# Optimization experiments

Hardware: AMD Instinct MI355X
Metric: run time of the kernel (lower is better)

Reference implementation:

```python
import jax, jax.numpy as jnp
import numpy as np

D = 512   # block_hidden_dim (also per-head dim in this module)
H = 8     # n_head
EPS_RENORM = 1e-13
LN_EPS = 1e-5

def setup_inputs() -> dict:
    key = jax.random.key(0)
    ks = jax.random.split(key, 10)
    B, L = 4, 1024
    std = np.sqrt(2.0 / (D * 2)).astype(np.float32)
    q = jax.random.normal(ks[0], (B, L, D), jnp.float32)
    k = jax.random.normal(ks[1], (B, L, D), jnp.float32)
    v = jax.random.normal(ks[2], (B, L, D), jnp.float32)
    mask = jax.random.randint(ks[3], (B, L, L), 0, 2, jnp.int32)
    Wq = jax.random.normal(ks[4], (H * D, D), jnp.float32) * std
    Wk = jax.random.normal(ks[5], (H * D, D), jnp.float32) * std
    Wv = jax.random.normal(ks[6], (H * D, D), jnp.float32) * std
    Wfc = jax.random.normal(ks[7], (D, H * D), jnp.float32) * np.sqrt(2.0 / (D + H * D)).astype(np.float32)
    bfc = jnp.zeros((D,), jnp.float32)
    gamma = jnp.ones((D,), jnp.float32)
    beta = jnp.zeros((D,), jnp.float32)
    return {"q": q, "mask": mask, "k": k, "v": v, "Wq": Wq, "Wk": Wk,
            "Wv": Wv, "Wfc": Wfc, "bfc": bfc, "gamma": gamma, "beta": beta}

def reference(q, mask, k, v, Wq, Wk, Wv, Wfc, bfc, gamma, beta):
    B, Lq, _ = q.shape
    residual = q
    # torch Linear: y = x @ W.T ; W reshaped to [H, D_out, D_in]
    qh = jnp.einsum('bqd,hed->bhqe', q, Wq.reshape(H, D, D))
    kh = jnp.einsum('bkd,hed->bhke', k, Wk.reshape(H, D, D))
    vh = jnp.einsum('bkd,hed->bhke', v, Wv.reshape(H, D, D))
    scores = jnp.einsum('bhqe,bhke->bhqk', qh, kh) / jnp.sqrt(jnp.float32(D))
    m = mask.astype(scores.dtype)[:, None, :, :]        # [B,1,Lq,Lk]
    # multiplicative-mask softmax + renormalization (allennlp masked_softmax)
    attn = jax.nn.softmax(scores * m, axis=-1)
    attn = attn * m
    attn = attn / (attn.sum(axis=-1, keepdims=True) + EPS_RENORM)
    out = jnp.einsum('bhqk,bhke->bhqe', attn, vh)       # [B,H,Lq,D]
    out = out.transpose(0, 2, 1, 3).reshape(B, Lq, H * D)  # head-major concat
    out = out @ Wfc.T + bfc                              # fc (dropout = eval no-op)
    x = out + residual
    mu = x.mean(axis=-1, keepdims=True)
    var = x.var(axis=-1, keepdims=True)
    out = (x - mu) / jnp.sqrt(var + LN_EPS) * gamma + beta
    attn_mean = attn.mean(axis=1)                        # mean over heads [B,Lq,Lk]
    return out, attn_mean
```

## Files before the change

### kernel.cpp

```cpp
#include <hip/hip_runtime.h>
#include <hip/hip_bf16.h>
#include <cmath>

typedef long long i64;
typedef unsigned short u16;
typedef __attribute__((ext_vector_type(8))) short short8;
typedef __attribute__((ext_vector_type(8))) unsigned short u16x8;
typedef __attribute__((ext_vector_type(4))) float f32x4;
typedef __attribute__((ext_vector_type(4))) int i32x4;

#define NB 4
#define NL 1024
#define ND 512
#define NH 8

__device__ __forceinline__ u16 f2bf(float f) {
    __hip_bfloat16 h = __float2bfloat16(f);
    return __builtin_bit_cast(unsigned short, h);
}
__device__ __forceinline__ float bf2f(u16 u) {
    return __builtin_bit_cast(float, (unsigned)u << 16);
}

typedef __attribute__((address_space(3))) u16* lds_u16p;
typedef const __attribute__((address_space(1))) u16* glb_u16p;
__device__ __forceinline__ void gl_lds16(const u16* g, u16* l) {
    __builtin_amdgcn_global_load_lds((glb_u16p)g, (lds_u16p)l, 16, 0, 0);
}

struct CvtArgs {
    const float* src[4];
    u16* dst[4];
};

__global__ __launch_bounds__(256) void cvt_multi_kernel(CvtArgs args, int n8)
{
    int i = blockIdx.x * 256 + threadIdx.x;
    if (i >= n8) return;
    const float* __restrict__ src = args.src[blockIdx.y];
    u16* __restrict__ dst = args.dst[blockIdx.y];
    float4 a = ((const float4*)src)[2 * i];
    float4 b = ((const float4*)src)[2 * i + 1];
    u16x8 o;
    o[0] = f2bf(a.x); o[1] = f2bf(a.y); o[2] = f2bf(a.z); o[3] = f2bf(a.w);
    o[4] = f2bf(b.x); o[5] = f2bf(b.y); o[6] = f2bf(b.z); o[7] = f2bf(b.w);
    *(u16x8*)&dst[8 * i] = o;
}

template <bool OUTBF, bool BIAS>
__global__ __launch_bounds__(256) void mfma_gemm(
    const u16* __restrict__ A, const u16* __restrict__ B,
    void* __restrict__ Cv, const float* __restrict__ bias,
    int K, int lda, int ldb, int ldc, float alpha,
    i64 a_s1, i64 a_s2, i64 b_s1, i64 b_s2, i64 c_s1, i64 c_s2)
{
    const int gxy  = gridDim.x * gridDim.y;
    const int nblk = gxy * gridDim.z;
    const int lin  = blockIdx.x + gridDim.x * blockIdx.y + gxy * blockIdx.z;
    const int swz  = (lin & 7) * (nblk >> 3) + (lin >> 3);
    const int bz   = swz / gxy;
    const int rxy  = swz - bz * gxy;
    const int by   = rxy / gridDim.x;
    const int bx   = rxy - by * gridDim.x;

    const int zh = bz >> 3, zl = bz & 7;
    A += (i64)zh * a_s1 + (i64)zl * a_s2;
    B += (i64)zh * b_s1 + (i64)zl * b_s2;
    const i64 coff = (i64)zh * c_s1 + (i64)zl * c_s2;

    __shared__ alignas(16) u16 As[128 * 64];
    __shared__ alignas(16) u16 Bs[128 * 64];

    const int tid  = threadIdx.x;
    const int lane = tid & 63;
    const int wave = tid >> 6;
    const int wr   = (wave >> 1) * 64;
    const int wc   = (wave & 1) * 64;
    const int lrow = lane & 15;
    const int kblk = lane >> 4;
    const int rsw  = (lrow & 7) * 8;
    const int m0   = by * 128;
    const int n0   = bx * 128;

    const int srow0 = wave * 32;
    const int lrel  = lane >> 3;
    const int grow  = srow0 + lrel;
    const int gchk  = ((lane & 7) ^ lrel) * 8;

    f32x4 acc[4][4];
    #pragma unroll
    for (int i = 0; i < 4; ++i)
        #pragma unroll
        for (int j = 0; j < 4; ++j)
            acc[i][j] = (f32x4){0.f, 0.f, 0.f, 0.f};

    for (int k0 = 0; k0 < K; k0 += 64) {
        #pragma unroll
        for (int j = 0; j < 4; ++j)
            gl_lds16(&A[(i64)(m0 + grow + 8 * j) * lda + k0 + gchk],
                     &As[(srow0 + 8 * j) * 64]);
        #pragma unroll
        for (int j = 0; j < 4; ++j)
            gl_lds16(&B[(i64)(n0 + grow + 8 * j) * ldb + k0 + gchk],
                     &Bs[(srow0 + 8 * j) * 64]);
        __syncthreads();

        #pragma unroll
        for (int kk = 0; kk < 2; ++kk) {
            short8 af[4], bg[4];
            #pragma unroll
            for (int m = 0; m < 4; ++m)
                af[m] = *(const short8*)&As[(wr + m * 16 + lrow) * 64 +
                                            (((kk * 32) + kblk * 8) ^ rsw)];
            #pragma unroll
            for (int n = 0; n < 4; ++n)
                bg[n] = *(const short8*)&Bs[(wc + n * 16 + lrow) * 64 +
                                            (((kk * 32) + kblk * 8) ^ rsw)];

            #pragma unroll
            for (int m = 0; m < 4; ++m)
                #pragma unroll
                for (int n = 0; n < 4; ++n)
                    acc[m][n] = __builtin_amdgcn_mfma_f32_16x16x32_bf16(
                        af[m], bg[n], acc[m][n], 0, 0, 0);
        }
        __syncthreads();
    }

    #pragma unroll
    for (int m = 0; m < 4; ++m) {
        #pragma unroll
        for (int n = 0; n < 4; ++n) {
            const int col = n0 + wc + n * 16 + lrow;
            float bv = BIAS ? bias[col] : 0.f;
            #pragma unroll
            for (int r = 0; r < 4; ++r) {
                const int row = m0 + wr + m * 16 + kblk * 4 + r;
                float val = acc[m][n][r] * alpha + bv;
                if (OUTBF)
                    ((u16*)Cv)[coff + (i64)row * ldc + col] = f2bf(val);
                else
                    ((float*)Cv)[coff + (i64)row * ldc + col] = val;
            }
        }
    }
}

template <int P>
__global__ __launch_bounds__(256) void reduce_fc_kernel(
    const float* __restrict__ part, const float* __restrict__ bias,
    float* __restrict__ outp, i64 pstride)
{
    i64 idx = (i64)blockIdx.x * 256 + threadIdx.x;
    float s = bias[idx & (ND - 1)];
    #pragma unroll
    for (int p = 0; p < P; ++p) s += part[(i64)p * pstride + idx];
    outp[idx] = s;
}

__device__ __forceinline__ float wave_red_sum(float v) {
    #pragma unroll
    for (int o = 32; o > 0; o >>= 1) v += __shfl_down(v, o, 64);
    return v;
}
__device__ __forceinline__ float wave_red_max(float v) {
    #pragma unroll
    for (int o = 32; o > 0; o >>= 1) v = fmaxf(v, __shfl_down(v, o, 64));
    return v;
}

__global__ __launch_bounds__(256) void softmax_fused_kernel(
    const u16* __restrict__ scores, const int* __restrict__ mask,
    u16* __restrict__ attn_bf, float* __restrict__ amean,
    i64 s_bstride, i64 m_bstride, i64 a_bstride, i64 o_bstride)
{
    const int qrow = blockIdx.x;
    const int bb   = blockIdx.y;
    const u16* sbase = scores + (i64)bb * s_bstride;
    const int* mrow = mask + (i64)bb * m_bstride + (i64)qrow * NL;
    u16* abase = attn_bf + (i64)bb * a_bstride;
    float* orow = amean + (i64)bb * o_bstride + (i64)qrow * NL;

    const int tid  = threadIdx.x;
    const int lane = tid & 63;
    const int wave = tid >> 6;

    __shared__ float wsum[4][NL];

    const int e0 = lane * 8;
    const int e1 = 512 + lane * 8;

    float mv[16];
    {
        i32x4 m0a = *(const i32x4*)&mrow[e0];
        i32x4 m0b = *(const i32x4*)&mrow[e0 + 4];
        i32x4 m1a = *(const i32x4*)&mrow[e1];
        i32x4 m1b = *(const i32x4*)&mrow[e1 + 4];
        #pragma unroll
        for (int i = 0; i < 4; ++i) {
            mv[i]      = (float)m0a[i];
            mv[4 + i]  = (float)m0b[i];
            mv[8 + i]  = (float)m1a[i];
            mv[12 + i] = (float)m1b[i];
        }
    }

    float msum[16];
    #pragma unroll
    for (int i = 0; i < 16; ++i) msum[i] = 0.f;

    #pragma unroll
    for (int hh = 0; hh < 2; ++hh) {
        const int h = wave + hh * 4;
        const u16* srow_p = sbase + ((i64)h * NL + qrow) * NL;
        u16* arow_p = abase + ((i64)h * NL + qrow) * NL;

        u16x8 s0 = *(const u16x8*)&srow_p[e0];
        u16x8 s1 = *(const u16x8*)&srow_p[e1];

        float zv[16];
        float lmax = -1e30f;
        #pragma unroll
        for (int i = 0; i < 8; ++i) {
            zv[i]     = bf2f(s0[i]) * mv[i];
            zv[8 + i] = bf2f(s1[i]) * mv[8 + i];
        }
        #pragma unroll
        for (int i = 0; i < 16; ++i) lmax = fmaxf(lmax, zv[i]);
        #pragma unroll
        for (int o = 1; o < 64; o <<= 1)
            lmax = fmaxf(lmax, __shfl_xor(lmax, o, 64));

        float e[16];
        float ls = 0.f;
        #pragma unroll
        for (int i = 0; i < 16; ++i) { e[i] = __expf(zv[i] - lmax); ls += e[i]; }
        #pragma unroll
        for (int o = 1; o < 64; o <<= 1) ls += __shfl_xor(ls, o, 64);

        float ls2 = 0.f;
        #pragma unroll
        for (int i = 0; i < 16; ++i) { e[i] = e[i] / ls * mv[i]; ls2 += e[i]; }
        #pragma unroll
        for (int o = 1; o < 64; o <<= 1) ls2 += __shfl_xor(ls2, o, 64);

        const float inv = 1.0f / (ls2 + 1e-13f);
        u16x8 o0, o1;
        #pragma unroll
        for (int i = 0; i < 8; ++i) {
            float p0 = e[i] * inv;
            float p1 = e[8 + i] * inv;
            o0[i] = f2bf(p0);
            o1[i] = f2bf(p1);
            msum[i]     += p0;
            msum[8 + i] += p1;
        }
        *(u16x8*)&arow_p[e0] = o0;
        *(u16x8*)&arow_p[e1] = o1;
    }

    #pragma unroll
    for (int i = 0; i < 8; ++i) {
        wsum[wave][e0 + i] = msum[i];
        wsum[wave][e1 + i] = msum[8 + i];
    }
    __syncthreads();
    #pragma unroll
    for (int i = 0; i < 4; ++i) {
        int j = tid + i * 256;
        orow[j] = (wsum[0][j] + wsum[1][j] + wsum[2][j] + wsum[3][j]) * 0.125f;
    }
}

__global__ __launch_bounds__(256) void ln_kernel(
    const float* __restrict__ fcout, const float* __restrict__ resid,
    const float* __restrict__ gamma, const float* __restrict__ beta,
    float* __restrict__ out)
{
    const int row = blockIdx.x;
    const float* xr = fcout + (i64)row * ND;
    const float* rr = resid + (i64)row * ND;
    const int tid = threadIdx.x;
    const int lane = tid & 63, wid = tid >> 6;
    __shared__ float red[8];

    float x0 = xr[tid] + rr[tid];
    float x1 = xr[tid + 256] + rr[tid + 256];
    float s  = x0 + x1;
    float s2 = x0 * x0 + x1 * x1;
    s  = wave_red_sum(s);
    s2 = wave_red_sum(s2);
    if (lane == 0) { red[wid] = s; red[4 + wid] = s2; }
    __syncthreads();
    const float S  = red[0] + red[1] + red[2] + red[3];
    const float S2 = red[4] + red[5] + red[6] + red[7];
    const float mu  = S * (1.0f / ND);
    const float var = S2 * (1.0f / ND) - mu * mu;
    const float inv = rsqrtf(var + 1e-5f);

    out[(i64)row * ND + tid]       = (x0 - mu) * inv * gamma[tid] + beta[tid];
    out[(i64)row * ND + tid + 256] = (x1 - mu) * inv * gamma[tid + 256] + beta[tid + 256];
}

template <bool BT, bool BIAS, bool ACC>
__global__ __launch_bounds__(256) void gemm_kernel(
    const float* __restrict__ A, const float* __restrict__ B,
    float* __restrict__ C, const float* __restrict__ bias,
    int M, int N, int K, int lda, int ldb, int ldc, float alpha)
{
    __shared__ float Asf[16][68];
    __shared__ float Bsf[16][68];
    const int tid = threadIdx.x;
    const int tx = tid & 15, ty = tid >> 4;
    const int m0 = blockIdx.y * 64, n0 = blockIdx.x * 64;
    float acc[4][4] = {};

    for (int k0 = 0; k0 < K; k0 += 16) {
        {
            int r = tid >> 2, kq = (tid & 3) << 2;
            float4 a = *reinterpret_cast<const float4*>(&A[(i64)(m0 + r) * lda + k0 + kq]);
            Asf[kq][r] = a.x; Asf[kq + 1][r] = a.y; Asf[kq + 2][r] = a.z; Asf[kq + 3][r] = a.w;
        }
        if (BT) {
            int r = tid >> 2, kq = (tid & 3) << 2;
            float4 b = *reinterpret_cast<const float4*>(&B[(i64)(n0 + r) * ldb + k0 + kq]);
            Bsf[kq][r] = b.x; Bsf[kq + 1][r] = b.y; Bsf[kq + 2][r] = b.z; Bsf[kq + 3][r] = b.w;
        } else {
            int kk = tid >> 4, n4 = (tid & 15) << 2;
            float4 b = *reinterpret_cast<const float4*>(&B[(i64)(k0 + kk) * ldb + n0 + n4]);
            *reinterpret_cast<float4*>(&Bsf[kk][n4]) = b;
        }
        __syncthreads();
        #pragma unroll
        for (int kk = 0; kk < 16; ++kk) {
            float4 a4 = *reinterpret_cast<const float4*>(&Asf[kk][ty << 2]);
            float4 b4 = *reinterpret_cast<const float4*>(&Bsf[kk][tx << 2]);
            float a[4] = {a4.x, a4.y, a4.z, a4.w};
            float b[4] = {b4.x, b4.y, b4.z, b4.w};
            #pragma unroll
            for (int i = 0; i < 4; ++i)
                #pragma unroll
                for (int j = 0; j < 4; ++j)
                    acc[i][j] = fmaf(a[i], b[j], acc[i][j]);
        }
        __syncthreads();
    }
    #pragma unroll
    for (int i = 0; i < 4; ++i) {
        int m = m0 + (ty << 2) + i;
        #pragma unroll
        for (int j = 0; j < 4; ++j) {
            int n = n0 + (tx << 2) + j;
            float val = acc[i][j] * alpha;
            if (BIAS) val += bias[n];
            i64 idx = (i64)m * ldc + n;
            if (ACC) C[idx] += val; else C[idx] = val;
        }
    }
}

__global__ __launch_bounds__(256) void softmax_kernel(
    float* __restrict__ attn, const int* __restrict__ mask)
{
    const int qrow = blockIdx.x;
    float* row = attn + (i64)qrow * NL;
    const int* mrow = mask + (i64)qrow * NL;
    const int tid = threadIdx.x;
    const int lane = tid & 63, wid = tid >> 6;
    __shared__ float red[4];

    float zv[4], mv[4];
    float lmax = -1e30f;
    #pragma unroll
    for (int i = 0; i < 4; ++i) {
        mv[i] = (float)mrow[tid + i * 256];
        zv[i] = row[tid + i * 256] * mv[i];
        lmax  = fmaxf(lmax, zv[i]);
    }
    float wv = wave_red_max(lmax);
    if (lane == 0) red[wid] = wv;
    __syncthreads();
    const float gmax = fmaxf(fmaxf(red[0], red[1]), fmaxf(red[2], red[3]));
    float e[4]; float ls = 0.f;
    #pragma unroll
    for (int i = 0; i < 4; ++i) { e[i] = __expf(zv[i] - gmax); ls += e[i]; }
    __syncthreads();
    wv = wave_red_sum(ls);
    if (lane == 0) red[wid] = wv;
    __syncthreads();
    const float S1 = red[0] + red[1] + red[2] + red[3];
    float ls2 = 0.f;
    #pragma unroll
    for (int i = 0; i < 4; ++i) { e[i] = e[i] / S1 * mv[i]; ls2 += e[i]; }
    __syncthreads();
    wv = wave_red_sum(ls2);
    if (lane == 0) red[wid] = wv;
    __syncthreads();
    const float S2 = red[0] + red[1] + red[2] + red[3];
    const float inv = 1.0f / (S2 + 1e-13f);
    #pragma unroll
    for (int i = 0; i < 4; ++i) row[tid + i * 256] = e[i] * inv;
}

__global__ __launch_bounds__(256) void mean_acc_kernel(
    const float* __restrict__ attn, float* __restrict__ out, int first)
{
    i64 idx = (i64)blockIdx.x * 256 + threadIdx.x;
    float v = attn[idx] * 0.125f;
    out[idx] = first ? v : (out[idx] + v);
}

extern "C" void kernel_launch(void* const* d_in, const int* in_sizes, int n_in,
                              void* d_out, int out_size, void* d_ws, size_t ws_size,
                              hipStream_t stream)
{
    const float* q     = (const float*)d_in[0];
    const int*   mask  = (const int*)  d_in[1];
    const float* k     = (const float*)d_in[2];
    const float* v     = (const float*)d_in[3];
    const float* Wq    = (const float*)d_in[4];
    const float* Wk    = (const float*)d_in[5];
    const float* Wv    = (const float*)d_in[6];
    const float* Wfc   = (const float*)d_in[7];
    const float* bfc   = (const float*)d_in[8];
    const float* gamma = (const float*)d_in[9];
    const float* beta  = (const float*)d_in[10];

    float* out       = (float*)d_out;
    float* attn_mean = out + (i64)NB * NL * ND;

    const float inv_sqrt_d = 0.04419417382415922f;
    const i64 LD  = (i64)NL * ND;
    const i64 LL  = (i64)NL * NL;
    const i64 ND2 = (i64)ND * ND;
    const i64 HLD = (i64)NH * LD;
    const i64 HLL = (i64)NH * LL;
    dim3 blk(256);

    const size_t MB = 1048576;

    if (ws_size >= 196 * MB) {
        char* wsb = (char*)d_ws;
        u16* Wq_bf  = (u16*)(wsb);
        u16* Wk_bf  = (u16*)(wsb + 4   * MB);
        u16* Wv_bf  = (u16*)(wsb + 8   * MB);
        u16* Wfc_bf = (u16*)(wsb + 12  * MB);
        u16* q_bf   = (u16*)(wsb + 16  * MB);
        u16* k_bf   = (u16*)(wsb + 20  * MB);
        u16* v_bf   = (u16*)(wsb + 24  * MB);
        u16* qh     = (u16*)(wsb + 28  * MB);
        u16* kh     = (u16*)(wsb + 60  * MB);
        u16* vht    = (u16*)(wsb + 92  * MB);
        u16* scores = (u16*)(wsb + 124 * MB);
        u16* attn_bf  = qh;
        u16* concat   = (u16*)(wsb + 124 * MB);
        float* fcpart = (float*)(wsb + 156 * MB);
        float* fcout  = (float*)(wsb + 188 * MB);

        {
            CvtArgs a;
            a.src[0] = Wq;  a.dst[0] = Wq_bf;
            a.src[1] = Wk;  a.dst[1] = Wk_bf;
            a.src[2] = Wv;  a.dst[2] = Wv_bf;
            a.src[3] = Wfc; a.dst[3] = Wfc_bf;
            cvt_multi_kernel<<<dim3(1024, 4), blk, 0, stream>>>(a, 262144);
        }
        {
            CvtArgs a;
            a.src[0] = q; a.dst[0] = q_bf;
            a.src[1] = k; a.dst[1] = k_bf;
            a.src[2] = v; a.dst[2] = v_bf;
            a.src[3] = q; a.dst[3] = q_bf;
            cvt_multi_kernel<<<dim3(1024, 3), blk, 0, stream>>>(a, 262144);
        }

        mfma_gemm<true, false><<<dim3(4, 8, 32), blk, 0, stream>>>(
            q_bf, Wq_bf, qh, nullptr, ND, ND, ND, ND, 1.0f,
            LD, 0, 0, ND2, HLD, LD);
        mfma_gemm<true, false><<<dim3(4, 8, 32), blk, 0, stream>>>(
            k_bf, Wk_bf, kh, nullptr, ND, ND, ND, ND, 1.0f,
            LD, 0, 0, ND2, HLD, LD);
        mfma_gemm<true, false><<<dim3(8, 4, 32), blk, 0, stream>>>(
            Wv_bf, v_bf, vht, nullptr, ND, ND, ND, NL, 1.0f,
            0, ND2, LD, 0, HLD, LD);

        mfma_gemm<true, false><<<dim3(8, 8, 32), blk, 0, stream>>>(
            qh, kh, scores, nullptr, ND, ND, ND, NL, inv_sqrt_d,
            HLD, LD, HLD, LD, HLL, LL);

        softmax_fused_kernel<<<dim3(NL, NB), blk, 0, stream>>>(
            scores, mask, attn_bf, attn_mean, HLL, LL, HLL, LL);

        mfma_gemm<true, false><<<dim3(4, 8, 32), blk, 0, stream>>>(
            attn_bf, vht, concat, nullptr, NL, NL, NL, NH * ND, 1.0f,
            HLL, LL, HLD, LD, (i64)NL * NH * ND, (i64)ND);

        mfma_gemm<false, false><<<dim3(4, 32, 4), blk, 0, stream>>>(
            concat, Wfc_bf, fcpart, nullptr, NL, NH * ND, NH * ND, ND, 1.0f,
            0, NL, 0, NL, 0, (i64)NB * NL * ND);
        reduce_fc_kernel<4><<<dim3(8192), blk, 0, stream>>>(
            fcpart, bfc, fcout, (i64)NB * NL * ND);

        ln_kernel<<<dim3(NB * NL), blk, 0, stream>>>(fcout, q, gamma, beta, out);

    } else if (ws_size >= 64 * MB) {
        char* wsb = (char*)d_ws;
        u16* Wq_bf  = (u16*)(wsb);
        u16* Wk_bf  = (u16*)(wsb + 4  * MB);
        u16* Wv_bf  = (u16*)(wsb + 8  * MB);
        u16* Wfc_bf = (u16*)(wsb + 12 * MB);
        u16* qb_bf  = (u16*)(wsb + 16 * MB);
        u16* kb_bf  = (u16*)(wsb + 17 * MB);
        u16* vb_bf  = (u16*)(wsb + 18 * MB);
        u16* qh     = (u16*)(wsb + 19 * MB);
        u16* kh     = (u16*)(wsb + 27 * MB);
        u16* vht    = (u16*)(wsb + 35 * MB);
        u16* scores = (u16*)(wsb + 43 * MB);
        u16* attn_bf  = qh;
        u16* concat   = (u16*)(wsb + 43 * MB);
        float* fcpart = (float*)(wsb + 51 * MB);
        float* fcout  = (float*)(wsb + 59 * MB);

        {
            CvtArgs a;
            a.src[0] = Wq;  a.dst[0] = Wq_bf;
            a.src[1] = Wk;  a.dst[1] = Wk_bf;
            a.src[2] = Wv;  a.dst[2] = Wv_bf;
            a.src[3] = Wfc; a.dst[3] = Wfc_bf;
            cvt_multi_kernel<<<dim3(1024, 4), blk, 0, stream>>>(a, 262144);
        }

        for (int b = 0; b < NB; ++b) {
            const float* qb = q + (i64)b * LD;
            const float* kb = k + (i64)b * LD;
            const float* vb = v + (i64)b * LD;
            const int* maskb = mask + (i64)b * LL;

            {
                CvtArgs a;
                a.src[0] = qb; a.dst[0] = qb_bf;
                a.src[1] = kb; a.dst[1] = kb_bf;
                a.src[2] = vb; a.dst[2] = vb_bf;
                a.src[3] = vb; a.dst[3] = vb_bf;
                cvt_multi_kernel<<<dim3(256, 3), blk, 0, stream>>>(a, 65536);
            }

            mfma_gemm<true, false><<<dim3(4, 8, NH), blk, 0, stream>>>(
                qb_bf, Wq_bf, qh, nullptr, ND, ND, ND, ND, 1.0f,
                0, 0, 0, ND2, 0, LD);
            mfma_gemm<true, false><<<dim3(4, 8, NH), blk, 0, stream>>>(
                kb_bf, Wk_bf, kh, nullptr, ND, ND, ND, ND, 1.0f,
                0, 0, 0, ND2, 0, LD);
            mfma_gemm<true, false><<<dim3(8, 4, NH), blk, 0, stream>>>(
                Wv_bf, vb_bf, vht, nullptr, ND, ND, ND, NL, 1.0f,
                0, ND2, 0, 0, 0, LD);

            mfma_gemm<true, false><<<dim3(8, 8, NH), blk, 0, stream>>>(
                qh, kh, scores, nullptr, ND, ND, ND, NL, inv_sqrt_d,
                0, LD, 0, LD, 0, LL);

            softmax_fused_kernel<<<dim3(NL, 1), blk, 0, stream>>>(
                scores, maskb, attn_bf, attn_mean + (i64)b * LL, 0, 0, 0, 0);

            mfma_gemm<true, false><<<dim3(4, 8, NH), blk, 0, stream>>>(
                attn_bf, vht, concat, nullptr, NL, NL, NL, NH * ND, 1.0f,
                0, LL, 0, LD, 0, (i64)ND);

            mfma_gemm<false, false><<<dim3(4, 8, 4), blk, 0, stream>>>(
                concat, Wfc_bf, fcpart, nullptr, NL, NH * ND, NH * ND, ND, 1.0f,
                0, NL, 0, NL, 0, LD);
            reduce_fc_kernel<4><<<dim3(2048), blk, 0, stream>>>(fcpart, bfc, fcout, LD);

            ln_kernel<<<dim3(NL), blk, 0, stream>>>(fcout, qb, gamma, beta, out + (i64)b * LD);
        }
    } else {
        float* ws = (float*)d_ws;
        float* qh_h   = ws;
        float* kh_h   = ws + LD;
        float* vh_h   = ws + 2 * LD;
        float* attn_h = ws + 3 * LD;
        float* headout = qh_h;
        float* fcout   = ws + 5 * LD;

        for (int b = 0; b < NB; ++b) {
            const float* qb = q + (i64)b * LD;
            const float* kb = k + (i64)b * LD;
            const float* vb = v + (i64)b * LD;
            const int* maskb = mask + (i64)b * LL;

            for (int h = 0; h < NH; ++h) {
                const i64 wofs = (i64)h * ND2;
                gemm_kernel<true, false, false><<<dim3(8, 16, 1), blk, 0, stream>>>(
                    qb, Wq + wofs, qh_h, nullptr, NL, ND, ND, ND, ND, ND, 1.0f);
                gemm_kernel<true, false, false><<<dim3(8, 16, 1), blk, 0, stream>>>(
                    kb, Wk + wofs, kh_h, nullptr, NL, ND, ND, ND, ND, ND, 1.0f);
                gemm_kernel<true, false, false><<<dim3(8, 16, 1), blk, 0, stream>>>(
                    vb, Wv + wofs, vh_h, nullptr, NL, ND, ND, ND, ND, ND, 1.0f);
                gemm_kernel<true, false, false><<<dim3(16, 16, 1), blk, 0, stream>>>(
                    qh_h, kh_h, attn_h, nullptr, NL, NL, ND, ND, ND, NL, inv_sqrt_d);
                softmax_kernel<<<dim3(NL), blk, 0, stream>>>(attn_h, maskb);
                mean_acc_kernel<<<dim3(4096), blk, 0, stream>>>(
                    attn_h, attn_mean + (i64)b * LL, h == 0 ? 1 : 0);
                gemm_kernel<false, false, false><<<dim3(8, 16, 1), blk, 0, stream>>>(
                    attn_h, vh_h, headout, nullptr, NL, ND, NL, NL, ND, ND, 1.0f);
                if (h == 0)
                    gemm_kernel<true, true, false><<<dim3(8, 16, 1), blk, 0, stream>>>(
                        headout, Wfc + (i64)h * ND, fcout, bfc, NL, ND, ND, ND, NH * ND, ND, 1.0f);
                else
                    gemm_kernel<true, false, true><<<dim3(8, 16, 1), blk, 0, stream>>>(
                        headout, Wfc + (i64)h * ND, fcout, nullptr, NL, ND, ND, ND, NH * ND, ND, 1.0f);
            }
            ln_kernel<<<dim3(NL), blk, 0, stream>>>(fcout, qb, gamma, beta, out + (i64)b * LD);
        }
    }
}
```

Before: 272.7 us.

## Double-buffer LDS tiles in bf16 MFMA GEMM to overlap loads with compute

New measurement: 259.6 us. 1.05x faster.

```diff
diff --git a/kernel.cpp b/kernel.cpp
--- a/kernel.cpp
+++ b/kernel.cpp
@@ -68,8 +68,8 @@
     B += (i64)zh * b_s1 + (i64)zl * b_s2;
     const i64 coff = (i64)zh * c_s1 + (i64)zl * c_s2;
 
-    __shared__ alignas(16) u16 As[128 * 64];
-    __shared__ alignas(16) u16 Bs[128 * 64];
+    __shared__ alignas(16) u16 As[2 * 128 * 64];
+    __shared__ alignas(16) u16 Bs[2 * 128 * 64];
 
     const int tid  = threadIdx.x;
     const int lane = tid & 63;
@@ -94,27 +94,48 @@
         for (int j = 0; j < 4; ++j)
             acc[i][j] = (f32x4){0.f, 0.f, 0.f, 0.f};
 
-    for (int k0 = 0; k0 < K; k0 += 64) {
-        #pragma unroll
-        for (int j = 0; j < 4; ++j)
-            gl_lds16(&A[(i64)(m0 + grow + 8 * j) * lda + k0 + gchk],
-                     &As[(srow0 + 8 * j) * 64]);
-        #pragma unroll
-        for (int j = 0; j < 4; ++j)
-            gl_lds16(&B[(i64)(n0 + grow + 8 * j) * ldb + k0 + gchk],
-                     &Bs[(srow0 + 8 * j) * 64]);
-        __syncthreads();
-
+    const int nt = K >> 6;
+
+    #pragma unroll
+    for (int j = 0; j < 4; ++j)
+        gl_lds16(&A[(i64)(m0 + grow + 8 * j) * lda + gchk],
+                 &As[(srow0 + 8 * j) * 64]);
+    #pragma unroll
+    for (int j = 0; j < 4; ++j)
+        gl_lds16(&B[(i64)(n0 + grow + 8 * j) * ldb + gchk],
+                 &Bs[(srow0 + 8 * j) * 64]);
+
+    int cur = 0;
+    for (int t = 0; t < nt; ++t) {
+        const int nxt = cur ^ 1;
+        if (t + 1 < nt) {
+            const int k0n = (t + 1) << 6;
+            #pragma unroll
+            for (int j = 0; j < 4; ++j)
+                gl_lds16(&A[(i64)(m0 + grow + 8 * j) * lda + k0n + gchk],
+                         &As[nxt * 8192 + (srow0 + 8 * j) * 64]);
+            #pragma unroll
+            for (int j = 0; j < 4; ++j)
+                gl_lds16(&B[(i64)(n0 + grow + 8 * j) * ldb + k0n + gchk],
+                         &Bs[nxt * 8192 + (srow0 + 8 * j) * 64]);
+            asm volatile("s_waitcnt vmcnt(8)" ::: "memory");
+        } else {
+            asm volatile("s_waitcnt vmcnt(0)" ::: "memory");
+        }
+        asm volatile("s_barrier" ::: "memory");
+
+        const u16* Ab = &As[cur * 8192];
+        const u16* Bb = &Bs[cur * 8192];
         #pragma unroll
         for (int kk = 0; kk < 2; ++kk) {
             short8 af[4], bg[4];
             #pragma unroll
             for (int m = 0; m < 4; ++m)
-                af[m] = *(const short8*)&As[(wr + m * 16 + lrow) * 64 +
+                af[m] = *(const short8*)&Ab[(wr + m * 16 + lrow) * 64 +
                                             (((kk * 32) + kblk * 8) ^ rsw)];
             #pragma unroll
             for (int n = 0; n < 4; ++n)
-                bg[n] = *(const short8*)&Bs[(wc + n * 16 + lrow) * 64 +
+                bg[n] = *(const short8*)&Bb[(wc + n * 16 + lrow) * 64 +
                                             (((kk * 32) + kblk * 8) ^ rsw)];
 
             #pragma unroll
@@ -124,7 +145,8 @@
                     acc[m][n] = __builtin_amdgcn_mfma_f32_16x16x32_bf16(
                         af[m], bg[n], acc[m][n], 0, 0, 0);
         }
-        __syncthreads();
+        asm volatile("s_barrier" ::: "memory");
+        cur = nxt;
     }
 
     #pragma unroll
@@ -161,11 +183,6 @@
 __device__ __forceinline__ float wave_red_sum(float v) {
     #pragma unroll
     for (int o = 32; o > 0; o >>= 1) v += __shfl_down(v, o, 64);
-    return v;
-}
-__device__ __forceinline__ float wave_red_max(float v) {
-    #pragma unroll
-    for (int o = 32; o > 0; o >>= 1) v = fmaxf(v, __shfl_down(v, o, 64));
     return v;
 }
 
@@ -357,6 +374,12 @@
             if (ACC) C[idx] += val; else C[idx] = val;
         }
     }
+}
+
+__device__ __forceinline__ float wave_red_max(float v) {
+    #pragma unroll
+    for (int o = 32; o > 0; o >>= 1) v = fmaxf(v, __shfl_down(v, o, 64));
+    return v;
 }
 
 __global__ __launch_bounds__(256) void softmax_kernel(
```
